# Kernel tuning notes

Hardware: AMD Instinct MI355X
Metric: run time of the kernel (lower is better)

The kernel has to match this reference:

```python
import jax, jax.numpy as jnp
import numpy as np
from jax import lax

# Production-scale dims: batch, seq_len, tag_size (incl. START/STOP tags)
B, S, T = 512, 512, 64


def setup_inputs() -> dict:
    key = jax.random.key(0)
    k1, k2, k3, k4 = jax.random.split(key, 4)
    feats = jax.random.normal(k1, (B, S, T), dtype=jnp.float32)
    # prefix-contiguous mask (module assumes mask[:, 0] == 1 and length-style masks)
    lengths = jax.random.randint(k2, (B,), S // 2, S + 1)
    mask = jnp.arange(S)[None, :] < lengths[:, None]  # (B, S) bool
    tags = jax.random.randint(k3, (B, S), 0, T - 2)  # gold tags exclude START/STOP
    transitions = jax.random.normal(k4, (T, T), dtype=jnp.float32) * 0.1
    return {"feats": feats, "mask": mask, "tags": tags, "transitions": transitions}


def _crf_nll(feats, transitions, mask, tags):
    b, s, t = feats.shape
    START, STOP = t - 2, t - 1  # START_TAG = -2, STOP_TAG = -1

    # ---- forward (log partition), matches _calculate_PZ ----
    # partition init: scores[0][:, START, :] = feats[:,0,:] + transitions[START, :]
    init = feats[:, 0, :] + transitions[START][None, :]  # (b, t)

    feats_t = jnp.swapaxes(feats, 0, 1)  # (s, b, t)
    mask_t = jnp.swapaxes(mask, 0, 1)    # (s, b)

    def step(partition, inp):
        f_t, m_t = inp  # (b, t), (b,)
        # cur_values[b, from, to] = feats_t[b, to] + transitions[from, to] + partition[b, from]
        cur = partition[:, :, None] + transitions[None, :, :] + f_t[:, None, :]
        new_p = jax.nn.logsumexp(cur, axis=1)  # reduce over 'from' -> (b, t)
        partition = jnp.where(m_t[:, None], new_p, partition)
        return partition, None

    partition, _ = lax.scan(step, init, (feats_t[1:], mask_t[1:]))

    # final transition to STOP
    final = jax.nn.logsumexp(partition[:, :, None] + transitions[None, :, :], axis=1)
    forward_score = final[:, STOP].sum()

    # ---- gold score, matches _score_sentence ----
    prev = jnp.concatenate(
        [jnp.full((b, 1), START, dtype=tags.dtype), tags[:, :-1]], axis=1
    )  # (b, s): previous tag, START at position 0
    emit = jnp.take_along_axis(feats, tags[:, :, None], axis=2)[:, :, 0]  # (b, s)
    tg_energy = emit + transitions[prev, tags]  # (b, s)
    gold = jnp.where(mask, tg_energy, jnp.zeros((), feats.dtype)).sum()
    lengths = mask.sum(axis=1).astype(jnp.int32)  # (b,)
    end_ids = jnp.take_along_axis(tags, (lengths - 1)[:, None].astype(tags.dtype), axis=1)[:, 0]
    gold = gold + transitions[end_ids, STOP].sum()

    # average_batch = False
    return forward_score - gold


def reference(feats, mask, tags, transitions):
    return _crf_nll(feats, transitions, mask, tags)
```

## Files before the change

kernel.cpp:

```cpp
#include <hip/hip_runtime.h>

#define BB 512
#define SS 512
#define TT 64
#define START_TAG 62
#define STOP_TAG 63

#define LOG2E 1.4426950408889634f
#define LN2   0.6931471805599453f

typedef _Float16 h2 __attribute__((ext_vector_type(2)));
typedef _Float16 h8 __attribute__((ext_vector_type(8)));
typedef float    f4 __attribute__((ext_vector_type(4)));

__device__ __forceinline__ h2 pkrtz(float a, float b) {
    return __builtin_bit_cast(h2, __builtin_amdgcn_cvt_pkrtz(a, b));
}
__device__ __forceinline__ f4 MF(h8 a, h8 b, f4 c) {
    return __builtin_amdgcn_mfma_f32_16x16x32_f16(a, b, c, 0, 0, 0);
}

__global__ void __launch_bounds__(192) crf_main(
    const float* __restrict__ feats, const int* __restrict__ mask,
    const int* __restrict__ tags, const float* __restrict__ trans,
    float* __restrict__ out)
{
    const int b    = blockIdx.x;
    const int tid  = threadIdx.x;
    const int wv   = tid >> 6;
    const int lane = tid & 63;

    const float* frow = feats + (size_t)b * SS * TT;
    const int*   mrow = mask + b * SS;

    __shared__ __align__(16) _Float16 febuf[2][8][TT];
    __shared__ __align__(16) float xbuf[TT];
    __shared__ __align__(16) float ybuf[TT];
    __shared__ int ks_sh[2];

    int cnt = 0;
    #pragma unroll
    for (int s = lane; s < SS; s += 64) cnt += (mrow[s] != 0);
    #pragma unroll
    for (int off = 32; off; off >>= 1) cnt += __shfl_xor(cnt, off);
    const int len = cnt;
    const int h   = len >> 1;

    float offs = 0.f;
    int   ksum = 0;

    if (wv < 2) {
        const bool isF = (wv == 0);
        const int g  = lane >> 4;
        const int cg = lane & 15;
        const int to_base   = 16 * (cg >> 2) + (cg & 3);
        const int nstep = isF ? h : (len - 1 - h);
        const int r0    = isF ? 0 : (len - 1);
        const int dir   = isF ? 1 : -1;
        _Float16 (*febw)[TT] = febuf[wv];

        h8 A[4][2];
        #pragma unroll
        for (int tt = 0; tt < 4; ++tt)
            #pragma unroll
            for (int kc = 0; kc < 2; ++kc)
                #pragma unroll
                for (int j = 0; j < 8; ++j) {
                    const int kt = 16 * g + 8 * kc + j;
                    const int ot = to_base + 4 * tt;
                    const int ix = isF ? (kt * TT + ot) : (ot * TT + kt);
                    A[tt][kc][j] =
                        (_Float16)__builtin_amdgcn_exp2f(trans[ix] * LOG2E);
                }

        h8 B0, B1;
        if (isF) {
            offs = frow[0] + trans[START_TAG * TT + 0];
            #pragma unroll
            for (int sl = 0; sl < 8; ++sl) {
                const int t0 = 16 * g + sl, t1 = t0 + 8;
                B0[sl] = (_Float16)__builtin_amdgcn_exp2f(
                    (trans[START_TAG * TT + t0] - offs) * LOG2E);
                B1[sl] = (_Float16)__builtin_amdgcn_exp2f(
                    (trans[START_TAG * TT + t1] - offs) * LOG2E);
            }
        } else {
            #pragma unroll
            for (int sl = 0; sl < 8; ++sl) {
                const int t0 = 16 * g + sl, t1 = t0 + 8;
                B0[sl] = (_Float16)__builtin_amdgcn_exp2f(
                    trans[t0 * TT + STOP_TAG] * LOG2E);
                B1[sl] = (_Float16)__builtin_amdgcn_exp2f(
                    trans[t1 * TT + STOP_TAG] * LOG2E);
            }
        }

        auto rowOf = [&](int idx) {
            int r = r0 + dir * idx;
            return r < 0 ? 0 : (r > SS - 1 ? SS - 1 : r);
        };

        float fr[8];
        #pragma unroll
        for (int j = 0; j < 8; ++j)
            fr[j] = frow[(size_t)rowOf(j) * TT + lane];
        #pragma unroll
        for (int j = 0; j < 4; ++j)
            febw[rowOf(j) & 7][lane] =
                (_Float16)__builtin_amdgcn_exp2f(fr[j] * LOG2E);
        h8 cL0, cL1, cL2, cL3, cH0, cH1, cH2, cH3;
        {
            const _Float16* p0 = &febw[rowOf(0) & 7][16 * g];
            const _Float16* p1 = &febw[rowOf(1) & 7][16 * g];
            const _Float16* p2 = &febw[rowOf(2) & 7][16 * g];
            const _Float16* p3 = &febw[rowOf(3) & 7][16 * g];
            cL0 = *(const h8*)p0; cH0 = *(const h8*)(p0 + 8);
            cL1 = *(const h8*)p1; cH1 = *(const h8*)(p1 + 8);
            cL2 = *(const h8*)p2; cH2 = *(const h8*)(p2 + 8);
            cL3 = *(const h8*)p3; cH3 = *(const h8*)(p3 + 8);
        }

        const f4 Z = {0.f, 0.f, 0.f, 0.f};
        auto STEP = [&](h8 feL, h8 feH) {
            const h8 a00 = A[0][0] * feL, a01 = A[0][1] * feH;
            const h8 a10 = A[1][0] * feL, a11 = A[1][1] * feH;
            const h8 a20 = A[2][0] * feL, a21 = A[2][1] * feH;
            const h8 a30 = A[3][0] * feL, a31 = A[3][1] * feH;
            const f4 d0 = MF(a01, B1, MF(a00, B0, Z));
            const f4 d1 = MF(a11, B1, MF(a10, B0, Z));
            const f4 d2 = MF(a21, B1, MF(a20, B0, Z));
            const f4 d3 = MF(a31, B1, MF(a30, B0, Z));
            const int eb = (__builtin_amdgcn_readfirstlane(
                                __float_as_int(d0[0])) >> 23) & 0xff;
            ksum += eb - 127;
            const float sc = __int_as_float((254 - eb) << 23);
            const h2 p0 = pkrtz(d0[0] * sc, d0[1] * sc);
            const h2 p1 = pkrtz(d0[2] * sc, d0[3] * sc);
            const h2 p2 = pkrtz(d1[0] * sc, d1[1] * sc);
            const h2 p3 = pkrtz(d1[2] * sc, d1[3] * sc);
            const h2 p4 = pkrtz(d2[0] * sc, d2[1] * sc);
            const h2 p5 = pkrtz(d2[2] * sc, d2[3] * sc);
            const h2 p6 = pkrtz(d3[0] * sc, d3[1] * sc);
            const h2 p7 = pkrtz(d3[2] * sc, d3[3] * sc);
            B0 = __builtin_shufflevector(
                     __builtin_shufflevector(p0, p1, 0, 1, 2, 3),
                     __builtin_shufflevector(p2, p3, 0, 1, 2, 3),
                     0, 1, 2, 3, 4, 5, 6, 7);
            B1 = __builtin_shufflevector(
                     __builtin_shufflevector(p4, p5, 0, 1, 2, 3),
                     __builtin_shufflevector(p6, p7, 0, 1, 2, 3),
                     0, 1, 2, 3, 4, 5, 6, 7);
        };

        int i = 0;
        for (; i + 3 < nstep; i += 4) {
            const float n0 = frow[(size_t)rowOf(i + 8)  * TT + lane];
            const float n1 = frow[(size_t)rowOf(i + 9)  * TT + lane];
            const float n2 = frow[(size_t)rowOf(i + 10) * TT + lane];
            const float n3 = frow[(size_t)rowOf(i + 11) * TT + lane];
            febw[rowOf(i + 4) & 7][lane] =
                (_Float16)__builtin_amdgcn_exp2f(fr[4] * LOG2E);
            febw[rowOf(i + 5) & 7][lane] =
                (_Float16)__builtin_amdgcn_exp2f(fr[5] * LOG2E);
            febw[rowOf(i + 6) & 7][lane] =
                (_Float16)__builtin_amdgcn_exp2f(fr[6] * LOG2E);
            febw[rowOf(i + 7) & 7][lane] =
                (_Float16)__builtin_amdgcn_exp2f(fr[7] * LOG2E);
            const _Float16* q0 = &febw[rowOf(i + 4) & 7][16 * g];
            const _Float16* q1 = &febw[rowOf(i + 5) & 7][16 * g];
            const _Float16* q2 = &febw[rowOf(i + 6) & 7][16 * g];
            const _Float16* q3 = &febw[rowOf(i + 7) & 7][16 * g];
            const h8 nL0 = *(const h8*)q0, nH0 = *(const h8*)(q0 + 8);
            const h8 nL1 = *(const h8*)q1, nH1 = *(const h8*)(q1 + 8);
            const h8 nL2 = *(const h8*)q2, nH2 = *(const h8*)(q2 + 8);
            const h8 nL3 = *(const h8*)q3, nH3 = *(const h8*)(q3 + 8);

            STEP(cL0, cH0); STEP(cL1, cH1); STEP(cL2, cH2); STEP(cL3, cH3);

            cL0 = nL0; cH0 = nH0; cL1 = nL1; cH1 = nH1;
            cL2 = nL2; cH2 = nH2; cL3 = nL3; cH3 = nH3;
            #pragma unroll
            for (int j = 0; j < 4; ++j) fr[j] = fr[j + 4];
            fr[4] = n0; fr[5] = n1; fr[6] = n2; fr[7] = n3;
        }

        const int rem = nstep - i;
        if (rem > 0) STEP(cL0, cH0);
        if (rem > 1) STEP(cL1, cH1);
        if (rem > 2) STEP(cL2, cH2);

        float* obuf = isF ? xbuf : ybuf;
        if (cg == 0) {
            #pragma unroll
            for (int sl = 0; sl < 8; ++sl) {
                obuf[16 * g + sl]     = (float)B0[sl];
                obuf[16 * g + 8 + sl] = (float)B1[sl];
            }
        }
        if (lane == 0) ks_sh[wv] = ksum;
    } else {
        const int* trow = tags + b * SS;
        int   gcnt = 0;
        float acc  = 0.f;
        for (int s = lane; s < SS; s += 64) {
            if (mrow[s] != 0) {
                ++gcnt;
                const int tag  = trow[s];
                const int prev = (s == 0) ? START_TAG : trow[s - 1];
                acc += frow[(size_t)s * TT + tag] + trans[prev * TT + tag];
            }
        }
        #pragma unroll
        for (int off = 32; off; off >>= 1) acc += __shfl_xor(acc, off);
        if (lane == 0) {
            const int end_id = trow[len - 1];
            atomicAdd(out, -(acc + trans[end_id * TT + STOP_TAG]));
        }
    }

    __syncthreads();

    if (wv == 0) {
        float z = xbuf[lane] * ybuf[lane] *
                  __builtin_amdgcn_exp2f(frow[(size_t)h * TT + lane] * LOG2E);
        #pragma unroll
        for (int off = 32; off; off >>= 1) z += __shfl_xor(z, off);
        if (lane == 0)
            atomicAdd(out, offs + (float)(ksum + ks_sh[1]) * LN2
                           + LN2 * __builtin_amdgcn_logf(z));
    }
}

extern "C" void kernel_launch(void* const* d_in, const int* in_sizes, int n_in,
                              void* d_out, int out_size, void* d_ws, size_t ws_size,
                              hipStream_t stream) {
    const float* feats = (const float*)d_in[0];
    const int*   mask  = (const int*)d_in[1];
    const int*   tags  = (const int*)d_in[2];
    const float* trans = (const float*)d_in[3];
    float* out = (float*)d_out;

    (void)hipMemsetAsync(out, 0, sizeof(float), stream);
    crf_main<<<BB, 192, 0, stream>>>(feats, mask, tags, trans, out);
}
```

Measured before the change: 186.0 us.

## Apply emission factor after MFMA to shorten per-step dependency chain

Restructures the forward/backward recurrence so the emission factor is multiplied onto the fp16 packed result after the matrix multiply, not into the A operand before it. The A matrices stay constant across steps, so the eight per-step packed multiplies before the MFMAs are removed from the critical path, and the MFMAs are reordered so four independent chains interleave. The boundary handling is shifted accordingly: initial vectors fold in the first and last emission, step counts change, the forward wave does a final extra transition step, and the meeting row's emission term is no longer read. It trades eight h2 multiplies after the conversion for fewer multiplies before the MFMA and better MFMA overlap, with some risk around length edge cases.

```diff
diff --git a/kernel.cpp b/kernel.cpp
--- a/kernel.cpp
+++ b/kernel.cpp
@@ -36,7 +36,7 @@
     __shared__ __align__(16) _Float16 febuf[2][8][TT];
     __shared__ __align__(16) float xbuf[TT];
     __shared__ __align__(16) float ybuf[TT];
-    __shared__ int ks_sh[2];
+    __shared__ int ks_sh;
 
     int cnt = 0;
     #pragma unroll
@@ -53,9 +53,9 @@
         const bool isF = (wv == 0);
         const int g  = lane >> 4;
         const int cg = lane & 15;
-        const int to_base   = 16 * (cg >> 2) + (cg & 3);
-        const int nstep = isF ? h : (len - 1 - h);
-        const int r0    = isF ? 0 : (len - 1);
+        const int to_base = 16 * (cg >> 2) + (cg & 3);
+        const int nstep = isF ? h : (len - h - 2);
+        const int base  = isF ? 1 : (len - 2);
         const int dir   = isF ? 1 : -1;
         _Float16 (*febw)[TT] = febuf[wv];
 
@@ -80,23 +80,24 @@
             for (int sl = 0; sl < 8; ++sl) {
                 const int t0 = 16 * g + sl, t1 = t0 + 8;
                 B0[sl] = (_Float16)__builtin_amdgcn_exp2f(
-                    (trans[START_TAG * TT + t0] - offs) * LOG2E);
+                    (frow[t0] + trans[START_TAG * TT + t0] - offs) * LOG2E);
                 B1[sl] = (_Float16)__builtin_amdgcn_exp2f(
-                    (trans[START_TAG * TT + t1] - offs) * LOG2E);
+                    (frow[t1] + trans[START_TAG * TT + t1] - offs) * LOG2E);
             }
         } else {
+            const float* fl = frow + (size_t)(len - 1) * TT;
             #pragma unroll
             for (int sl = 0; sl < 8; ++sl) {
                 const int t0 = 16 * g + sl, t1 = t0 + 8;
                 B0[sl] = (_Float16)__builtin_amdgcn_exp2f(
-                    trans[t0 * TT + STOP_TAG] * LOG2E);
+                    (fl[t0] + trans[t0 * TT + STOP_TAG]) * LOG2E);
                 B1[sl] = (_Float16)__builtin_amdgcn_exp2f(
-                    trans[t1 * TT + STOP_TAG] * LOG2E);
+                    (fl[t1] + trans[t1 * TT + STOP_TAG]) * LOG2E);
             }
         }
 
         auto rowOf = [&](int idx) {
-            int r = r0 + dir * idx;
+            int r = base + dir * idx;
             return r < 0 ? 0 : (r > SS - 1 ? SS - 1 : r);
         };
 
@@ -122,14 +123,14 @@
 
         const f4 Z = {0.f, 0.f, 0.f, 0.f};
         auto STEP = [&](h8 feL, h8 feH) {
-            const h8 a00 = A[0][0] * feL, a01 = A[0][1] * feH;
-            const h8 a10 = A[1][0] * feL, a11 = A[1][1] * feH;
-            const h8 a20 = A[2][0] * feL, a21 = A[2][1] * feH;
-            const h8 a30 = A[3][0] * feL, a31 = A[3][1] * feH;
-            const f4 d0 = MF(a01, B1, MF(a00, B0, Z));
-            const f4 d1 = MF(a11, B1, MF(a10, B0, Z));
-            const f4 d2 = MF(a21, B1, MF(a20, B0, Z));
-            const f4 d3 = MF(a31, B1, MF(a30, B0, Z));
+            f4 d0 = MF(A[0][0], B0, Z);
+            f4 d1 = MF(A[1][0], B0, Z);
+            f4 d2 = MF(A[2][0], B0, Z);
+            f4 d3 = MF(A[3][0], B0, Z);
+            d0 = MF(A[0][1], B1, d0);
+            d1 = MF(A[1][1], B1, d1);
+            d2 = MF(A[2][1], B1, d2);
+            d3 = MF(A[3][1], B1, d3);
             const int eb = (__builtin_amdgcn_readfirstlane(
                                 __float_as_int(d0[0])) >> 23) & 0xff;
             ksum += eb - 127;
@@ -142,13 +143,21 @@
             const h2 p5 = pkrtz(d2[2] * sc, d2[3] * sc);
             const h2 p6 = pkrtz(d3[0] * sc, d3[1] * sc);
             const h2 p7 = pkrtz(d3[2] * sc, d3[3] * sc);
+            const h2 q0 = p0 * __builtin_shufflevector(feL, feL, 0, 1);
+            const h2 q1 = p1 * __builtin_shufflevector(feL, feL, 2, 3);
+            const h2 q2 = p2 * __builtin_shufflevector(feL, feL, 4, 5);
+            const h2 q3 = p3 * __builtin_shufflevector(feL, feL, 6, 7);
+            const h2 q4 = p4 * __builtin_shufflevector(feH, feH, 0, 1);
+            const h2 q5 = p5 * __builtin_shufflevector(feH, feH, 2, 3);
+            const h2 q6 = p6 * __builtin_shufflevector(feH, feH, 4, 5);
+            const h2 q7 = p7 * __builtin_shufflevector(feH, feH, 6, 7);
             B0 = __builtin_shufflevector(
-                     __builtin_shufflevector(p0, p1, 0, 1, 2, 3),
-                     __builtin_shufflevector(p2, p3, 0, 1, 2, 3),
+                     __builtin_shufflevector(q0, q1, 0, 1, 2, 3),
+                     __builtin_shufflevector(q2, q3, 0, 1, 2, 3),
                      0, 1, 2, 3, 4, 5, 6, 7);
             B1 = __builtin_shufflevector(
-                     __builtin_shufflevector(p4, p5, 0, 1, 2, 3),
-                     __builtin_shufflevector(p6, p7, 0, 1, 2, 3),
+                     __builtin_shufflevector(q4, q5, 0, 1, 2, 3),
+                     __builtin_shufflevector(q6, q7, 0, 1, 2, 3),
                      0, 1, 2, 3, 4, 5, 6, 7);
         };
 
@@ -166,14 +175,14 @@
                 (_Float16)__builtin_amdgcn_exp2f(fr[6] * LOG2E);
             febw[rowOf(i + 7) & 7][lane] =
                 (_Float16)__builtin_amdgcn_exp2f(fr[7] * LOG2E);
-            const _Float16* q0 = &febw[rowOf(i + 4) & 7][16 * g];
-            const _Float16* q1 = &febw[rowOf(i + 5) & 7][16 * g];
-            const _Float16* q2 = &febw[rowOf(i + 6) & 7][16 * g];
-            const _Float16* q3 = &febw[rowOf(i + 7) & 7][16 * g];
-            const h8 nL0 = *(const h8*)q0, nH0 = *(const h8*)(q0 + 8);
-            const h8 nL1 = *(const h8*)q1, nH1 = *(const h8*)(q1 + 8);
-            const h8 nL2 = *(const h8*)q2, nH2 = *(const h8*)(q2 + 8);
-            const h8 nL3 = *(const h8*)q3, nH3 = *(const h8*)(q3 + 8);
+            const _Float16* q0p = &febw[rowOf(i + 4) & 7][16 * g];
+            const _Float16* q1p = &febw[rowOf(i + 5) & 7][16 * g];
+            const _Float16* q2p = &febw[rowOf(i + 6) & 7][16 * g];
+            const _Float16* q3p = &febw[rowOf(i + 7) & 7][16 * g];
+            const h8 nL0 = *(const h8*)q0p, nH0 = *(const h8*)(q0p + 8);
+            const h8 nL1 = *(const h8*)q1p, nH1 = *(const h8*)(q1p + 8);
+            const h8 nL2 = *(const h8*)q2p, nH2 = *(const h8*)(q2p + 8);
+            const h8 nL3 = *(const h8*)q3p, nH3 = *(const h8*)(q3p + 8);
 
             STEP(cL0, cH0); STEP(cL1, cH1); STEP(cL2, cH2); STEP(cL3, cH3);
 
@@ -189,22 +198,43 @@
         if (rem > 1) STEP(cL1, cH1);
         if (rem > 2) STEP(cL2, cH2);
 
-        float* obuf = isF ? xbuf : ybuf;
-        if (cg == 0) {
-            #pragma unroll
-            for (int sl = 0; sl < 8; ++sl) {
-                obuf[16 * g + sl]     = (float)B0[sl];
-                obuf[16 * g + 8 + sl] = (float)B1[sl];
-            }
-        }
-        if (lane == 0) ks_sh[wv] = ksum;
+        if (isF) {
+            f4 d0 = MF(A[0][0], B0, Z);
+            f4 d1 = MF(A[1][0], B0, Z);
+            f4 d2 = MF(A[2][0], B0, Z);
+            f4 d3 = MF(A[3][0], B0, Z);
+            d0 = MF(A[0][1], B1, d0);
+            d1 = MF(A[1][1], B1, d1);
+            d2 = MF(A[2][1], B1, d2);
+            d3 = MF(A[3][1], B1, d3);
+            const int eb = (__builtin_amdgcn_readfirstlane(
+                                __float_as_int(d0[0])) >> 23) & 0xff;
+            ksum += eb - 127;
+            const float sc = __int_as_float((254 - eb) << 23);
+            if (cg == 0) {
+                #pragma unroll
+                for (int r = 0; r < 4; ++r) {
+                    xbuf[16 * g + 0 * 4 + r] = d0[r] * sc;
+                    xbuf[16 * g + 1 * 4 + r] = d1[r] * sc;
+                    xbuf[16 * g + 2 * 4 + r] = d2[r] * sc;
+                    xbuf[16 * g + 3 * 4 + r] = d3[r] * sc;
+                }
+            }
+        } else {
+            if (cg == 0) {
+                #pragma unroll
+                for (int sl = 0; sl < 8; ++sl) {
+                    ybuf[16 * g + sl]     = (float)B0[sl];
+                    ybuf[16 * g + 8 + sl] = (float)B1[sl];
+                }
+            }
+            if (lane == 0) ks_sh = ksum;
+        }
     } else {
         const int* trow = tags + b * SS;
-        int   gcnt = 0;
-        float acc  = 0.f;
+        float acc = 0.f;
         for (int s = lane; s < SS; s += 64) {
             if (mrow[s] != 0) {
-                ++gcnt;
                 const int tag  = trow[s];
                 const int prev = (s == 0) ? START_TAG : trow[s - 1];
                 acc += frow[(size_t)s * TT + tag] + trans[prev * TT + tag];
@@ -221,12 +251,11 @@
     __syncthreads();
 
     if (wv == 0) {
-        float z = xbuf[lane] * ybuf[lane] *
-                  __builtin_amdgcn_exp2f(frow[(size_t)h * TT + lane] * LOG2E);
+        float z = xbuf[lane] * ybuf[lane];
         #pragma unroll
         for (int off = 32; off; off >>= 1) z += __shfl_xor(z, off);
         if (lane == 0)
-            atomicAdd(out, offs + (float)(ksum + ks_sh[1]) * LN2
+            atomicAdd(out, offs + (float)(ksum + ks_sh) * LN2
                            + LN2 * __builtin_amdgcn_logf(z));
     }
 }
```

Result: faster. 166.8 us (-10.3%).
